# Kernel optimization log

Hardware: AMD Instinct MI355X
Metric: run time of the kernel (lower is better)

Reference implementation:

```python
import jax, jax.numpy as jnp
import numpy as np

EMBED = 1024
HEADS = 16
HEAD_DIM = EMBED // HEADS


def setup_inputs() -> dict:
    key = jax.random.key(0)
    ks = jax.random.split(key, 8)
    B, S, D = 4, 2048, EMBED
    s = 1.0 / np.sqrt(D)
    return {
        "values": jax.random.normal(ks[0], (B, S, D), jnp.float32),
        "keys": jax.random.normal(ks[1], (B, S, D), jnp.float32),
        "query": jax.random.normal(ks[2], (B, S, D), jnp.float32),
        "Wv": jax.random.normal(ks[3], (D, D), jnp.float32) * s,
        "Wk": jax.random.normal(ks[4], (D, D), jnp.float32) * s,
        "Wq": jax.random.normal(ks[5], (D, D), jnp.float32) * s,
        "Wo": jax.random.normal(ks[6], (D, D), jnp.float32) * s,
        "bo": jax.random.normal(ks[7], (D,), jnp.float32) * 0.01,
    }


def reference(values, keys, query, Wv, Wk, Wq, Wo, bo):
    N, Lq, D = query.shape
    Lk = keys.shape[1]
    Lv = values.shape[1]
    # torch Linear: y = x @ W.T
    v = (values @ Wv.T).reshape(N, Lv, HEADS, HEAD_DIM)
    k = (keys @ Wk.T).reshape(N, Lk, HEADS, HEAD_DIM)
    q = (query @ Wq.T).reshape(N, Lq, HEADS, HEAD_DIM)
    energy = jnp.einsum('nqhd,nkhd->nhqk', q, k)
    # NOTE: module scales by 1/sqrt(embed_size), not 1/sqrt(head_dim)
    attn = jax.nn.softmax(energy / jnp.sqrt(jnp.float32(D)), axis=3)
    out = jnp.einsum('nhql,nlhd->nqhd', attn, v).reshape(N, Lq, D)
    return out @ Wo.T + bo
```

## Files before the change

kernel.cpp:

```cpp
#include <hip/hip_runtime.h>
#include <cstdint>
#include <cstddef>


typedef unsigned short ushortT;
typedef __bf16 bf16x8 __attribute__((ext_vector_type(8)));
typedef _Float16 f16x4 __attribute__((ext_vector_type(4)));
typedef _Float16 f16x2 __attribute__((ext_vector_type(2)));
typedef float f32x4 __attribute__((ext_vector_type(4)));
typedef unsigned int u32x2 __attribute__((ext_vector_type(2)));
typedef unsigned short us4 __attribute__((ext_vector_type(4)));
typedef unsigned short us8 __attribute__((ext_vector_type(8)));

#define S_LEN 2048
#define NB 4
#define NH 16
#define HD 64
#define DMODEL 1024
#define MTOT 8192
#define WSZ 1048576

#define AS1 __attribute__((address_space(1)))
#define AS3 __attribute__((address_space(3)))

__device__ __forceinline__ ushortT f2b(float f) {
  unsigned x = __builtin_bit_cast(unsigned, f);
  x += 0x7fffu + ((x >> 16) & 1u);
  return (ushortT)(x >> 16);
}

__device__ __forceinline__ unsigned rne_pack(unsigned lo, unsigned hi) {
  lo += 0x7fffu + ((lo >> 16) & 1u);
  hi += 0x7fffu + ((hi >> 16) & 1u);
  return __builtin_amdgcn_perm(hi, lo, 0x07060302u);
}

__device__ __forceinline__ f32x4 mfma_bf16(bf16x8 a, bf16x8 b, f32x4 c) {
  return __builtin_amdgcn_mfma_f32_16x16x32_bf16(a, b, c, 0, 0, 0);
}
__device__ __forceinline__ f32x4 mfma16_f16(f16x4 a, f16x4 b, f32x4 c) {
  return __builtin_amdgcn_mfma_f32_16x16x16f16(a, b, c, 0, 0, 0);
}

__device__ __forceinline__ void gl2lds16(const ushortT* g, ushortT* l) {
  __builtin_amdgcn_global_load_lds((const AS1 void*)g, (AS3 void*)l, 16, 0, 0);
}

__global__ __launch_bounds__(256) void convert_w_kernel(
    const float* __restrict__ wq, const float* __restrict__ wk,
    const float* __restrict__ wv, const float* __restrict__ wo,
    ushortT* __restrict__ dst) {
  const float* s;
  switch (blockIdx.y) {
    case 0: s = wq; break;
    case 1: s = wk; break;
    case 2: s = wv; break;
    default: s = wo; break;
  }
  ushortT* d = dst + (size_t)blockIdx.y * WSZ;
  const size_t i = ((size_t)blockIdx.x * 256 + threadIdx.x) * 8;
  uint4 w0 = *(const uint4*)(s + i);
  uint4 w1 = *(const uint4*)(s + i + 4);
  uint4 pk;
  pk.x = rne_pack(w0.x, w0.y);
  pk.y = rne_pack(w0.z, w0.w);
  pk.z = rne_pack(w1.x, w1.y);
  pk.w = rne_pack(w1.z, w1.w);
  *(uint4*)(d + i) = pk;
}

template <int VT_MODE, bool A_F32, bool OUT_F32, bool HAS_BIAS, int ASTR>
__device__ __forceinline__ void gemm_bt_tile(const void* __restrict__ A,
                                             const ushortT* __restrict__ W,
                                             const float* __restrict__ bias,
                                             void* __restrict__ C, float oscale,
                                             ushortT* __restrict__ As,
                                             ushortT* __restrict__ Bs) {
  constexpr int K = 1024, N = 1024;
  static_assert(A_F32 || ASTR == 32, "gl2lds A staging requires linear rows");
  const int tid = threadIdx.x;
  const int wave = tid >> 6, lane = tid & 63, quad = lane >> 4, l16 = lane & 15;
  const int wm = wave & 1, wn = wave >> 1;
  const int by = blockIdx.x, bx = blockIdx.y;

  const size_t Aoff = (size_t)by * 128 * K;
  const ushortT* Wb = W + (size_t)bx * 128 * K;

  const f32x4 fz = {0.f, 0.f, 0.f, 0.f};
  f32x4 acc[4][4];
#pragma unroll
  for (int mi = 0; mi < 4; mi++)
#pragma unroll
    for (int ni = 0; ni < 4; ni++) acc[mi][ni] = fz;

  for (int kt = 0; kt < K; kt += 32) {
    __syncthreads();
#pragma unroll
    for (int i = 0; i < 2; ++i) {
      const int cb = (wave * 2 + i) * 64;
      const int c = cb + lane;
      const int m = c >> 2, ko = c & 3;
      gl2lds16(Wb + (size_t)m * K + kt + ko * 8, Bs + (size_t)cb * 8);
    }
    if (A_F32) {
#pragma unroll
      for (int j = 0; j < 2; ++j) {
        const int c = tid + j * 256;
        const int m = c >> 2, ko = c & 3;
        const float* ap = (const float*)A + Aoff + (size_t)m * K + kt + ko * 8;
        uint4 w0 = *(const uint4*)ap;
        uint4 w1 = *(const uint4*)(ap + 4);
        uint4 pk;
        pk.x = rne_pack(w0.x, w0.y);
        pk.y = rne_pack(w0.z, w0.w);
        pk.z = rne_pack(w1.x, w1.y);
        pk.w = rne_pack(w1.z, w1.w);
        *(uint4*)(As + (size_t)m * ASTR + ko * 8) = pk;
      }
    } else {
#pragma unroll
      for (int i = 0; i < 2; ++i) {
        const int cb = (wave * 2 + i) * 64;
        const int c = cb + lane;
        const int m = c >> 2, ko = c & 3;
        gl2lds16((const ushortT*)A + Aoff + (size_t)m * K + kt + ko * 8,
                 As + (size_t)cb * 8);
      }
    }
    __syncthreads();

    bf16x8 af[4], bfr[4];
#pragma unroll
    for (int mi = 0; mi < 4; mi++)
      af[mi] =
          *(const bf16x8*)(As + (wm * 64 + mi * 16 + l16) * ASTR + quad * 8);
#pragma unroll
    for (int ni = 0; ni < 4; ni++)
      bfr[ni] = *(const bf16x8*)(Bs + (wn * 64 + ni * 16 + l16) * 32 + quad * 8);
#pragma unroll
    for (int mi = 0; mi < 4; mi++)
#pragma unroll
      for (int ni = 0; ni < 4; ni++)
        acc[mi][ni] = mfma_bf16(af[mi], bfr[ni], acc[mi][ni]);
  }

#pragma unroll
  for (int mi = 0; mi < 4; mi++) {
    const int row0 = by * 128 + wm * 64 + mi * 16 + quad * 4;
#pragma unroll
    for (int ni = 0; ni < 4; ni++) {
      const int col = bx * 128 + wn * 64 + ni * 16 + l16;
      const float bv = HAS_BIAS ? bias[col] : 0.f;
      if (VT_MODE == 0) {
#pragma unroll
        for (int i = 0; i < 4; i++) {
          const size_t idx = (size_t)(row0 + i) * N + col;
          const float val = acc[mi][ni][i] * oscale + bv;
          if (OUT_F32)
            ((float*)C)[idx] = val;
          else
            ((ushortT*)C)[idx] = f2b(val);
        }
      } else {
        const int h = col >> 6, dd = col & 63;
        const int bb = row0 >> 11, s0 = row0 & (S_LEN - 1);
        u32x2 pk;
        pk[0] = __builtin_bit_cast(
            unsigned, __builtin_amdgcn_cvt_pkrtz(acc[mi][ni][0], acc[mi][ni][1]));
        pk[1] = __builtin_bit_cast(
            unsigned, __builtin_amdgcn_cvt_pkrtz(acc[mi][ni][2], acc[mi][ni][3]));
        *(u32x2*)((ushortT*)C + ((size_t)((bb * NH + h) * HD + dd) << 11) + s0) =
            pk;
      }
    }
  }
}

__global__ __launch_bounds__(256) void qkv_proj_kernel(
    const float* __restrict__ vals, const float* __restrict__ keys,
    const float* __restrict__ qry, const ushortT* __restrict__ wcat,
    ushortT* __restrict__ qb, ushortT* __restrict__ kb,
    ushortT* __restrict__ vtb) {
  __shared__ alignas(16) ushortT As[128 * 40];
  __shared__ alignas(16) ushortT Bs[128 * 32];
  const int z = blockIdx.z;
  const float QSC = 1.44269504088896f / 32.0f;
  if (z == 0)
    gemm_bt_tile<0, true, false, false, 40>(qry, wcat, nullptr, qb, QSC, As,
                                            Bs);
  else if (z == 1)
    gemm_bt_tile<0, true, false, false, 40>(keys, wcat + WSZ, nullptr, kb,
                                            1.0f, As, Bs);
  else
    gemm_bt_tile<1, true, false, false, 40>(vals, wcat + 2 * WSZ, nullptr, vtb,
                                            1.0f, As, Bs);
}

__global__ __launch_bounds__(256) void out_proj_kernel(
    const ushortT* __restrict__ ain, const ushortT* __restrict__ wo,
    const float* __restrict__ bo, float* __restrict__ out) {
  __shared__ alignas(16) ushortT As[128 * 32];
  __shared__ alignas(16) ushortT Bs[128 * 32];
  gemm_bt_tile<0, false, true, true, 32>(ain, wo, bo, out, 1.0f, As, Bs);
}

__global__ __launch_bounds__(256) void attn_kernel(
    const ushortT* __restrict__ qb, const ushortT* __restrict__ kb,
    const ushortT* __restrict__ vtb, ushortT* __restrict__ ab) {
  __shared__ alignas(16) ushortT Ks[128 * 72];
  __shared__ alignas(16) ushortT Vts[64 * 136];

  const int tid = threadIdx.x;
  const int wave = tid >> 6, lane = tid & 63, quad = lane >> 4, l16 = lane & 15;
  const int bh = blockIdx.x, qt = blockIdx.y, b = bh >> 4, h = bh & 15;

  bf16x8 qf[2][2];
#pragma unroll
  for (int mi = 0; mi < 2; mi++)
#pragma unroll
    for (int kq = 0; kq < 2; kq++) {
      const int qrow = qt * 128 + wave * 32 + mi * 16 + l16;
      qf[mi][kq] = *(const bf16x8*)(qb + (size_t)(b * S_LEN + qrow) * DMODEL +
                                    h * HD + kq * 32 + quad * 8);
    }

  const f32x4 fz = {0.f, 0.f, 0.f, 0.f};
  f32x4 osum[4][2];
#pragma unroll
  for (int ni = 0; ni < 4; ni++)
#pragma unroll
    for (int mi = 0; mi < 2; mi++) osum[ni][mi] = fz;
  float lsum[2] = {0.f, 0.f};

  us8 kreg[4], vreg[4];
  auto issue_loads = [&](int t) {
#pragma unroll
    for (int p = 0; p < 4; p++) {
      const int r = (tid >> 3) + p * 32, c = (tid & 7) * 8;
      kreg[p] = *(const us8*)(kb + (size_t)(b * S_LEN + t * 128 + r) * DMODEL +
                              h * HD + c);
    }
#pragma unroll
    for (int p = 0; p < 4; p++) {
      const int r = (tid >> 4) + p * 16, c = (tid & 15) * 8;
      vreg[p] = *(const us8*)(vtb + (size_t)((b * NH + h) * HD + r) * S_LEN +
                              t * 128 + c);
    }
  };
  issue_loads(0);

  for (int t = 0; t < 16; ++t) {
    __syncthreads();
#pragma unroll
    for (int p = 0; p < 4; p++) {
      const int r = (tid >> 3) + p * 32, c = (tid & 7) * 8;
      *(us8*)(Ks + r * 72 + c) = kreg[p];
    }
#pragma unroll
    for (int p = 0; p < 4; p++) {
      const int r = (tid >> 4) + p * 16, c = (tid & 15) * 8;
      *(us8*)(Vts + r * 136 + c) = vreg[p];
    }
    if (t < 15) issue_loads(t + 1);
    __syncthreads();

#pragma unroll
    for (int h2 = 0; h2 < 2; ++h2) {
      f32x4 sacc[4][2];
#pragma unroll
      for (int mt = 0; mt < 4; mt++)
#pragma unroll
        for (int mi = 0; mi < 2; mi++) sacc[mt][mi] = fz;
      __builtin_amdgcn_s_setprio(1);
#pragma unroll
      for (int kq = 0; kq < 2; kq++)
#pragma unroll
        for (int mt = 0; mt < 4; mt++) {
          bf16x8 kf = *(const bf16x8*)(Ks + ((h2 * 4 + mt) * 16 + l16) * 72 +
                                       kq * 32 + quad * 8);
#pragma unroll
          for (int mi = 0; mi < 2; mi++)
            sacc[mt][mi] = mfma_bf16(kf, qf[mi][kq], sacc[mt][mi]);
        }
      __builtin_amdgcn_s_setprio(0);

      u32x2 pf[4][2];
#pragma unroll
      for (int mt = 0; mt < 4; mt++)
#pragma unroll
        for (int mi = 0; mi < 2; mi++) {
          const float e0 = __builtin_amdgcn_exp2f(sacc[mt][mi][0]);
          const float e1 = __builtin_amdgcn_exp2f(sacc[mt][mi][1]);
          const float e2 = __builtin_amdgcn_exp2f(sacc[mt][mi][2]);
          const float e3 = __builtin_amdgcn_exp2f(sacc[mt][mi][3]);
          lsum[mi] += (e0 + e1) + (e2 + e3);
          pf[mt][mi][0] =
              __builtin_bit_cast(unsigned, __builtin_amdgcn_cvt_pkrtz(e0, e1));
          pf[mt][mi][1] =
              __builtin_bit_cast(unsigned, __builtin_amdgcn_cvt_pkrtz(e2, e3));
        }

      __builtin_amdgcn_s_setprio(1);
#pragma unroll
      for (int s = 0; s < 4; ++s)
#pragma unroll
        for (int ni = 0; ni < 4; ni++) {
          f16x4 vf = *(const f16x4*)(Vts + (ni * 16 + l16) * 136 +
                                     (h2 * 4 + s) * 16 + quad * 4);
#pragma unroll
          for (int mi = 0; mi < 2; mi++)
            osum[ni][mi] =
                mfma16_f16(vf, __builtin_bit_cast(f16x4, pf[s][mi]), osum[ni][mi]);
        }
      __builtin_amdgcn_s_setprio(0);
    }
  }

#pragma unroll
  for (int mi = 0; mi < 2; mi++) {
    float s = lsum[mi];
    s += __shfl_xor(s, 16, 64);
    s += __shfl_xor(s, 32, 64);
    lsum[mi] = 1.0f / s;
  }

#pragma unroll
  for (int mi = 0; mi < 2; mi++) {
    const int qrow = qt * 128 + wave * 32 + mi * 16 + l16;
#pragma unroll
    for (int ni = 0; ni < 4; ni++) {
      us4 pk;
#pragma unroll
      for (int i = 0; i < 4; i++) pk[i] = f2b(osum[ni][mi][i] * lsum[mi]);
      *(us4*)(ab + (size_t)(b * S_LEN + qrow) * DMODEL + h * HD + ni * 16 +
              quad * 4) = pk;
    }
  }
}

extern "C" void kernel_launch(void* const* d_in, const int* in_sizes, int n_in,
                              void* d_out, int out_size, void* d_ws,
                              size_t ws_size, hipStream_t stream) {
  const float* vals = (const float*)d_in[0];
  const float* keys = (const float*)d_in[1];
  const float* qry = (const float*)d_in[2];
  const float* Wv = (const float*)d_in[3];
  const float* Wk = (const float*)d_in[4];
  const float* Wq = (const float*)d_in[5];
  const float* Wo = (const float*)d_in[6];
  const float* bo = (const float*)d_in[7];
  float* out = (float*)d_out;

  ushortT* ws = (ushortT*)d_ws;
  const size_t E = (size_t)MTOT * DMODEL;
  ushortT* qbuf = ws;
  ushortT* kbuf = ws + E;
  ushortT* vtb = ws + 2 * E;
  ushortT* wcat = ws + 3 * E;
  ushortT* abuf = qbuf;

  dim3 blk(256, 1, 1);
  convert_w_kernel<<<dim3(512, 4), blk, 0, stream>>>(Wq, Wk, Wv, Wo, wcat);
  qkv_proj_kernel<<<dim3(64, 8, 3), blk, 0, stream>>>(vals, keys, qry, wcat,
                                                      qbuf, kbuf, vtb);
  attn_kernel<<<dim3(64, 16), blk, 0, stream>>>(qbuf, kbuf, vtb, abuf);
  out_proj_kernel<<<dim3(64, 8), blk, 0, stream>>>(abuf, wcat + 3 * WSZ, bo,
                                                   out);
}
```

Baseline: 365.4 us.

## Pre-convert activations to bf16 and use 8-wave out-projection GEMM

```diff
diff --git a/kernel.cpp b/kernel.cpp
--- a/kernel.cpp
+++ b/kernel.cpp
@@ -6,7 +6,6 @@
 typedef unsigned short ushortT;
 typedef __bf16 bf16x8 __attribute__((ext_vector_type(8)));
 typedef _Float16 f16x4 __attribute__((ext_vector_type(4)));
-typedef _Float16 f16x2 __attribute__((ext_vector_type(2)));
 typedef float f32x4 __attribute__((ext_vector_type(4)));
 typedef unsigned int u32x2 __attribute__((ext_vector_type(2)));
 typedef unsigned short us4 __attribute__((ext_vector_type(4)));
@@ -69,7 +68,29 @@
   *(uint4*)(d + i) = pk;
 }
 
-template <int VT_MODE, bool A_F32, bool OUT_F32, bool HAS_BIAS, int ASTR>
+__global__ __launch_bounds__(256) void convert_x_kernel(
+    const float* __restrict__ vals, const float* __restrict__ keys,
+    const float* __restrict__ qry, ushortT* __restrict__ dst) {
+  const float* s;
+  switch (blockIdx.y) {
+    case 0: s = vals; break;
+    case 1: s = keys; break;
+    default: s = qry; break;
+  }
+  ushortT* d = dst + (size_t)blockIdx.y * ((size_t)MTOT * DMODEL);
+  const size_t i = ((size_t)blockIdx.x * 256 + threadIdx.x) * 8;
+  uint4 w0 = *(const uint4*)(s + i);
+  uint4 w1 = *(const uint4*)(s + i + 4);
+  uint4 pk;
+  pk.x = rne_pack(w0.x, w0.y);
+  pk.y = rne_pack(w0.z, w0.w);
+  pk.z = rne_pack(w1.x, w1.y);
+  pk.w = rne_pack(w1.z, w1.w);
+  *(uint4*)(d + i) = pk;
+}
+
+template <int VT_MODE, bool A_F32, bool OUT_F32, bool HAS_BIAS, int ASTR,
+          int NW>
 __device__ __forceinline__ void gemm_bt_tile(const void* __restrict__ A,
                                              const ushortT* __restrict__ W,
                                              const float* __restrict__ bias,
@@ -77,6 +98,9 @@
                                              ushortT* __restrict__ As,
                                              ushortT* __restrict__ Bs) {
   constexpr int K = 1024, N = 1024;
+  constexpr int NI = (NW == 4) ? 4 : 2;
+  constexpr int CPT = 8 / NW;
+  static_assert(!A_F32 || NW == 4, "f32 A staging implemented for 4 waves");
   static_assert(A_F32 || ASTR == 32, "gl2lds A staging requires linear rows");
   const int tid = threadIdx.x;
   const int wave = tid >> 6, lane = tid & 63, quad = lane >> 4, l16 = lane & 15;
@@ -87,17 +111,17 @@
   const ushortT* Wb = W + (size_t)bx * 128 * K;
 
   const f32x4 fz = {0.f, 0.f, 0.f, 0.f};
-  f32x4 acc[4][4];
+  f32x4 acc[4][NI];
 #pragma unroll
   for (int mi = 0; mi < 4; mi++)
 #pragma unroll
-    for (int ni = 0; ni < 4; ni++) acc[mi][ni] = fz;
+    for (int ni = 0; ni < NI; ni++) acc[mi][ni] = fz;
 
   for (int kt = 0; kt < K; kt += 32) {
     __syncthreads();
 #pragma unroll
-    for (int i = 0; i < 2; ++i) {
-      const int cb = (wave * 2 + i) * 64;
+    for (int i = 0; i < CPT; ++i) {
+      const int cb = (wave * CPT + i) * 64;
       const int c = cb + lane;
       const int m = c >> 2, ko = c & 3;
       gl2lds16(Wb + (size_t)m * K + kt + ko * 8, Bs + (size_t)cb * 8);
@@ -119,8 +143,8 @@
       }
     } else {
 #pragma unroll
-      for (int i = 0; i < 2; ++i) {
-        const int cb = (wave * 2 + i) * 64;
+      for (int i = 0; i < CPT; ++i) {
+        const int cb = (wave * CPT + i) * 64;
         const int c = cb + lane;
         const int m = c >> 2, ko = c & 3;
         gl2lds16((const ushortT*)A + Aoff + (size_t)m * K + kt + ko * 8,
@@ -129,18 +153,19 @@
     }
     __syncthreads();
 
-    bf16x8 af[4], bfr[4];
+    bf16x8 af[4], bfr[NI];
 #pragma unroll
     for (int mi = 0; mi < 4; mi++)
       af[mi] =
           *(const bf16x8*)(As + (wm * 64 + mi * 16 + l16) * ASTR + quad * 8);
 #pragma unroll
-    for (int ni = 0; ni < 4; ni++)
-      bfr[ni] = *(const bf16x8*)(Bs + (wn * 64 + ni * 16 + l16) * 32 + quad * 8);
+    for (int ni = 0; ni < NI; ni++)
+      bfr[ni] = *(const bf16x8*)(Bs + (wn * (NI * 16) + ni * 16 + l16) * 32 +
+                                 quad * 8);
 #pragma unroll
     for (int mi = 0; mi < 4; mi++)
 #pragma unroll
-      for (int ni = 0; ni < 4; ni++)
+      for (int ni = 0; ni < NI; ni++)
         acc[mi][ni] = mfma_bf16(af[mi], bfr[ni], acc[mi][ni]);
   }
 
@@ -148,8 +173,8 @@
   for (int mi = 0; mi < 4; mi++) {
     const int row0 = by * 128 + wm * 64 + mi * 16 + quad * 4;
 #pragma unroll
-    for (int ni = 0; ni < 4; ni++) {
-      const int col = bx * 128 + wn * 64 + ni * 16 + l16;
+    for (int ni = 0; ni < NI; ni++) {
+      const int col = bx * 128 + wn * (NI * 16) + ni * 16 + l16;
       const float bv = HAS_BIAS ? bias[col] : 0.f;
       if (VT_MODE == 0) {
 #pragma unroll
@@ -176,6 +201,26 @@
   }
 }
 
+__global__ __launch_bounds__(256) void qkv_proj_bf16_kernel(
+    const ushortT* __restrict__ xb, const ushortT* __restrict__ wcat,
+    ushortT* __restrict__ qb, ushortT* __restrict__ kb,
+    ushortT* __restrict__ vtb) {
+  __shared__ alignas(16) ushortT As[128 * 32];
+  __shared__ alignas(16) ushortT Bs[128 * 32];
+  const size_t E = (size_t)MTOT * DMODEL;
+  const int z = blockIdx.z;
+  const float QSC = 1.44269504088896f / 32.0f;
+  if (z == 0)
+    gemm_bt_tile<0, false, false, false, 32, 4>(xb + 2 * E, wcat, nullptr, qb,
+                                                QSC, As, Bs);
+  else if (z == 1)
+    gemm_bt_tile<0, false, false, false, 32, 4>(xb + E, wcat + WSZ, nullptr,
+                                                kb, 1.0f, As, Bs);
+  else
+    gemm_bt_tile<1, false, false, false, 32, 4>(xb, wcat + 2 * WSZ, nullptr,
+                                                vtb, 1.0f, As, Bs);
+}
+
 __global__ __launch_bounds__(256) void qkv_proj_kernel(
     const float* __restrict__ vals, const float* __restrict__ keys,
     const float* __restrict__ qry, const ushortT* __restrict__ wcat,
@@ -186,22 +231,22 @@
   const int z = blockIdx.z;
   const float QSC = 1.44269504088896f / 32.0f;
   if (z == 0)
-    gemm_bt_tile<0, true, false, false, 40>(qry, wcat, nullptr, qb, QSC, As,
-                                            Bs);
+    gemm_bt_tile<0, true, false, false, 40, 4>(qry, wcat, nullptr, qb, QSC, As,
+                                               Bs);
   else if (z == 1)
-    gemm_bt_tile<0, true, false, false, 40>(keys, wcat + WSZ, nullptr, kb,
-                                            1.0f, As, Bs);
+    gemm_bt_tile<0, true, false, false, 40, 4>(keys, wcat + WSZ, nullptr, kb,
+                                               1.0f, As, Bs);
   else
-    gemm_bt_tile<1, true, false, false, 40>(vals, wcat + 2 * WSZ, nullptr, vtb,
-                                            1.0f, As, Bs);
-}
-
-__global__ __launch_bounds__(256) void out_proj_kernel(
+    gemm_bt_tile<1, true, false, false, 40, 4>(vals, wcat + 2 * WSZ, nullptr,
+                                               vtb, 1.0f, As, Bs);
+}
+
+__global__ __launch_bounds__(512) void out_proj_kernel(
     const ushortT* __restrict__ ain, const ushortT* __restrict__ wo,
     const float* __restrict__ bo, float* __restrict__ out) {
   __shared__ alignas(16) ushortT As[128 * 32];
   __shared__ alignas(16) ushortT Bs[128 * 32];
-  gemm_bt_tile<0, false, true, true, 32>(ain, wo, bo, out, 1.0f, As, Bs);
+  gemm_bt_tile<0, false, true, true, 32, 8>(ain, wo, bo, out, 1.0f, As, Bs);
 }
 
 __global__ __launch_bounds__(256) void attn_kernel(
@@ -357,13 +402,22 @@
   ushortT* kbuf = ws + E;
   ushortT* vtb = ws + 2 * E;
   ushortT* wcat = ws + 3 * E;
+  ushortT* xb = ws + 3 * E + 4 * (size_t)WSZ;
   ushortT* abuf = qbuf;
+
+  const size_t need = (6 * E + 4 * (size_t)WSZ) * sizeof(ushortT);
 
   dim3 blk(256, 1, 1);
   convert_w_kernel<<<dim3(512, 4), blk, 0, stream>>>(Wq, Wk, Wv, Wo, wcat);
-  qkv_proj_kernel<<<dim3(64, 8, 3), blk, 0, stream>>>(vals, keys, qry, wcat,
-                                                      qbuf, kbuf, vtb);
+  if (ws_size >= need) {
+    convert_x_kernel<<<dim3(4096, 3), blk, 0, stream>>>(vals, keys, qry, xb);
+    qkv_proj_bf16_kernel<<<dim3(64, 8, 3), blk, 0, stream>>>(xb, wcat, qbuf,
+                                                             kbuf, vtb);
+  } else {
+    qkv_proj_kernel<<<dim3(64, 8, 3), blk, 0, stream>>>(vals, keys, qry, wcat,
+                                                        qbuf, kbuf, vtb);
+  }
   attn_kernel<<<dim3(64, 16), blk, 0, stream>>>(qbuf, kbuf, vtb, abuf);
-  out_proj_kernel<<<dim3(64, 8), blk, 0, stream>>>(abuf, wcat + 3 * WSZ, bo,
-                                                   out);
-}
+  out_proj_kernel<<<dim3(64, 8), dim3(512, 1, 1), 0, stream>>>(
+      abuf, wcat + 3 * WSZ, bo, out);
+}
```

New measurement: 344.3 us. 5.8% less time.
